# Kernel optimization log

Measured on AMD Instinct MI355X. Metric: run time of the kernel, lower is better.

## Reference

```python
import jax, jax.numpy as jnp
import numpy as np

MAX_P = 20
MAX_N = 50
FDIM = 256
SCALE = 0.08
STEPS = 3


def _grid_sample_border(feat_hwc, grid):
    # feat_hwc: [B,H,W,C]; grid: [B,Q,2] normalized xy in [-1,1]
    # Bilinear grid_sample, padding_mode='border', align_corners=False (matches torch).
    B, H, W, C = feat_hwc.shape

    def one(fm, g):  # fm [H,W,C], g [Q,2]
        ix = jnp.clip(((g[:, 0] + 1.0) * W - 1.0) * 0.5, 0.0, W - 1.0)
        iy = jnp.clip(((g[:, 1] + 1.0) * H - 1.0) * 0.5, 0.0, H - 1.0)
        x0f = jnp.floor(ix); y0f = jnp.floor(iy)
        wx = (ix - x0f)[:, None]; wy = (iy - y0f)[:, None]
        x0 = x0f.astype(jnp.int32); y0 = y0f.astype(jnp.int32)
        x1 = jnp.minimum(x0 + 1, W - 1); y1 = jnp.minimum(y0 + 1, H - 1)
        f00 = fm[y0, x0]; f01 = fm[y0, x1]  # [Q,C]
        f10 = fm[y1, x0]; f11 = fm[y1, x1]
        top = f00 * (1.0 - wx) + f01 * wx
        bot = f10 * (1.0 - wx) + f11 * wx
        return top * (1.0 - wy) + bot * wy

    return jax.vmap(one)(feat_hwc, grid)


def setup_inputs() -> dict:
    key = jax.random.key(0)
    ks = jax.random.split(key, 12)
    d = {
        'p2': jax.random.normal(ks[0], (4, 256, 256, 256), jnp.float32),
        'p4': jax.random.normal(ks[1], (4, 256, 64, 64), jnp.float32),
        'iw1': jax.random.normal(ks[2], (16384, 512), jnp.float32) * 0.01,
        'ib1': jnp.zeros((512,), jnp.float32),
        'iw2': jax.random.normal(ks[3], (512, 1024), jnp.float32) * 0.04,
        'ib2': jnp.zeros((1024,), jnp.float32),
        'iw3': jax.random.normal(ks[4], (1024, 2000), jnp.float32) * 0.03,
        'ib3': jnp.zeros((2000,), jnp.float32),
        'rw1': jax.random.normal(ks[5], (258, 256), jnp.float32) * 0.06,
        'rb1': jnp.zeros((256,), jnp.float32),
        'rw2': jax.random.normal(ks[6], (256, 128), jnp.float32) * 0.06,
        'rb2': jnp.zeros((128,), jnp.float32),
        'rw3': jax.random.normal(ks[7], (128, 2), jnp.float32) * 0.09,
        'rb3': jnp.zeros((2,), jnp.float32),
        'vw1': jax.random.normal(ks[8], (100, 128), jnp.float32) * 0.1,
        'vb1': jnp.zeros((128,), jnp.float32),
        'vw2': jax.random.normal(ks[9], (128, 1), jnp.float32) * 0.09,
        'vb2': jnp.zeros((1,), jnp.float32),
    }
    return d


def reference(p2, p4, iw1, ib1, iw2, ib2, iw3, ib3,
              rw1, rb1, rw2, rb2, rw3, rb3, vw1, vb1, vw2, vb2):
    B = p4.shape[0]
    # AdaptiveAvgPool2d(8) on 64x64 -> mean over 8x8 blocks
    pooled = p4.reshape(B, FDIM, 8, 8, 8, 8).mean(axis=(3, 5))  # [B,C,8,8]
    flat = pooled.reshape(B, -1)  # [B, C*64]
    h = jax.nn.relu(flat @ iw1 + ib1)
    h = jax.nn.relu(h @ iw2 + ib2)
    init_polygons = jax.nn.sigmoid(h @ iw3 + ib3).reshape(B, MAX_P, MAX_N, 2)

    feat_hwc = jnp.transpose(p2, (0, 2, 3, 1))  # [B,H,W,C]
    polygons = init_polygons
    for _ in range(STEPS):
        coords = polygons.reshape(B, -1, 2)           # [B,Q,2] in [0,1]
        grid = coords * 2.0 - 1.0
        sampled = _grid_sample_border(feat_hwc, grid)  # [B,Q,C]
        inp = jnp.concatenate([sampled, coords], axis=-1)  # [B,Q,C+2]
        r = jax.nn.relu(inp @ rw1 + rb1)
        r = jax.nn.relu(r @ rw2 + rb2)
        disp = jnp.tanh(r @ rw3 + rb3).reshape(B, MAX_P, MAX_N, 2)
        bad = ~jnp.all(jnp.isfinite(disp))
        disp = jnp.where(bad, 0.0,
                         jnp.clip(disp * SCALE, -2.0 * SCALE, 2.0 * SCALE))
        polygons = jnp.clip(polygons + disp, 0.0, 1.0)

    poly_flat = polygons.reshape(B * MAX_P, MAX_N * 2)
    v = jax.nn.relu(poly_flat @ vw1 + vb1)
    validity = jax.nn.sigmoid(v @ vw2 + vb2).reshape(B, MAX_P)
    return polygons, validity, init_polygons
```

## Files before the change

kernel.cpp:

```cpp
#include <hip/hip_runtime.h>
#include <hip/hip_fp16.h>
#include <math.h>

#define WS_FLAT 0
#define WS_PART 65536
#define WS_H1   (65536 + 524288)
#define WS_H2   (WS_H1 + 2048)
#define WS_POLY (WS_H2 + 4096)
#define WS_P2T  1048576

__global__ void __launch_bounds__(256) transpose_k(const float* __restrict__ in,
                                                   __half* __restrict__ out) {
    __shared__ float t[64][65];
    int tile = blockIdx.x;
    int b  = tile >> 12;
    int ct = (tile >> 10) & 3;
    int xt = tile & 1023;
    int c0 = ct << 6, yx0 = xt << 6;
    int tid = threadIdx.x;

    int jv = (tid & 15) << 2;
    int i0 = tid >> 4;
    const float* ip = in + (((size_t)(b * 256 + c0)) << 16) + yx0;
    #pragma unroll
    for (int ii = i0; ii < 64; ii += 16) {
        float4 v = *(const float4*)(ip + ((size_t)ii << 16) + jv);
        t[jv + 0][ii] = v.x; t[jv + 1][ii] = v.y;
        t[jv + 2][ii] = v.z; t[jv + 3][ii] = v.w;
    }
    __syncthreads();

    int cl = (tid & 7) << 3;
    #pragma unroll
    for (int jj = tid >> 3; jj < 64; jj += 32) {
        union { __half h[8]; float4 f; } u;
        #pragma unroll
        for (int q = 0; q < 8; ++q) u.h[q] = __float2half(t[jj][cl + q]);
        *(float4*)(out + ((size_t)b << 24) + ((size_t)(yx0 + jj) << 8) + c0 + cl) = u.f;
    }
}

__global__ void pool_k(const float* __restrict__ p4, float* __restrict__ flat) {
    int o = blockIdx.x * blockDim.x + threadIdx.x;
    int b = o >> 14;
    int c = (o >> 6) & 255;
    int ij = o & 63;
    int i = ij >> 3, j = ij & 7;
    const float* base = p4 + (((size_t)(b * 256 + c) * 64 + i * 8) * 64 + j * 8);
    float s = 0.f;
    #pragma unroll
    for (int u = 0; u < 8; ++u) {
        const float4* r = (const float4*)(base + u * 64);
        float4 a = r[0], bb = r[1];
        s += a.x + a.y + a.z + a.w + bb.x + bb.y + bb.z + bb.w;
    }
    flat[o] = s * (1.0f / 64.0f);
}

__global__ void g1a_k(const float* __restrict__ flat, const float* __restrict__ iw1,
                      float* __restrict__ part) {
    __shared__ float sf[4][64];
    int tid = threadIdx.x;
    int kbase = blockIdx.x * 64;
    if (tid < 256) sf[tid >> 6][tid & 63] = flat[(tid >> 6) * 16384 + kbase + (tid & 63)];
    __syncthreads();
    float a0 = 0.f, a1 = 0.f, a2 = 0.f, a3 = 0.f;
    for (int k = 0; k < 64; ++k) {
        float w = iw1[(size_t)(kbase + k) * 512 + tid];
        a0 = fmaf(sf[0][k], w, a0);
        a1 = fmaf(sf[1][k], w, a1);
        a2 = fmaf(sf[2][k], w, a2);
        a3 = fmaf(sf[3][k], w, a3);
    }
    float* pp = part + (size_t)blockIdx.x * 2048;
    pp[tid] = a0; pp[512 + tid] = a1; pp[1024 + tid] = a2; pp[1536 + tid] = a3;
}

__global__ void g1b_k(const float* __restrict__ part, const float* __restrict__ ib1,
                      float* __restrict__ h1) {
    __shared__ float red[8][32];
    int tid = threadIdx.x;
    int cc = tid >> 5, oo = tid & 31;
    int o = blockIdx.x * 32 + oo;
    float s = 0.f;
    for (int i = 0; i < 32; ++i)
        s += part[(size_t)(cc + 8 * i) * 2048 + o];
    red[cc][oo] = s;
    __syncthreads();
    if (cc == 0) {
        float t = 0.f;
        #pragma unroll
        for (int c2 = 0; c2 < 8; ++c2) t += red[c2][oo];
        t += ib1[o & 511];
        h1[o] = fmaxf(t, 0.f);
    }
}

__global__ void g2_k(const float* __restrict__ h1, const float* __restrict__ iw2,
                     const float* __restrict__ ib2, float* __restrict__ h2) {
    __shared__ float sh[512];
    __shared__ float red[4][64];
    int tid = threadIdx.x;
    int b = blockIdx.x >> 4, jt = blockIdx.x & 15;
    sh[tid] = h1[b * 512 + tid];
    sh[tid + 256] = h1[b * 512 + 256 + tid];
    __syncthreads();
    int j = (jt << 6) + (tid & 63);
    int kc = tid >> 6;
    float acc = 0.f;
    for (int k = kc * 128; k < kc * 128 + 128; ++k)
        acc = fmaf(sh[k], iw2[(size_t)k * 1024 + j], acc);
    red[kc][tid & 63] = acc;
    __syncthreads();
    if (kc == 0) {
        float t = red[0][tid] + red[1][tid] + red[2][tid] + red[3][tid] + ib2[j];
        h2[b * 1024 + j] = fmaxf(t, 0.f);
    }
}

__global__ void g3_k(const float* __restrict__ h2, const float* __restrict__ iw3,
                     const float* __restrict__ ib3, float* __restrict__ out_init,
                     float* __restrict__ poly) {
    __shared__ float sh[1024];
    __shared__ float red[4][64];
    int tid = threadIdx.x;
    int b = blockIdx.x >> 5, jt = blockIdx.x & 31;
    const float* h = h2 + b * 1024;
    sh[tid] = h[tid]; sh[tid + 256] = h[tid + 256];
    sh[tid + 512] = h[tid + 512]; sh[tid + 768] = h[tid + 768];
    __syncthreads();
    int j = (jt << 6) + (tid & 63);
    int kc = tid >> 6;
    float acc = 0.f;
    if (j < 2000) {
        for (int k = kc * 256; k < kc * 256 + 256; ++k)
            acc = fmaf(sh[k], iw3[(size_t)k * 2000 + j], acc);
    }
    red[kc][tid & 63] = acc;
    __syncthreads();
    if (kc == 0 && j < 2000) {
        float t = red[0][tid] + red[1][tid] + red[2][tid] + red[3][tid] + ib3[j];
        float s = 1.f / (1.f + expf(-t));
        int o = b * 2000 + j;
        out_init[o] = s;
        poly[o] = s;
    }
}

__global__ void __launch_bounds__(256) step_k(
    const __half* __restrict__ p2th,
    const float* __restrict__ rw1, const float* __restrict__ rb1,
    const float* __restrict__ rw2, const float* __restrict__ rb2,
    const float* __restrict__ rw3, const float* __restrict__ rb3,
    float* __restrict__ poly) {
    __shared__ __align__(16) float s_inp[258 * 16];
    __shared__ __align__(16) float s_r1[256 * 16];
    __shared__ __align__(16) float s_r2[128 * 16];
    int tid = threadIdx.x;
    int pt0 = blockIdx.x * 16;

    {
        int ch2 = (tid & 127) << 1;
        int pgg = tid >> 7;
        float v0[8], v1[8];
        #pragma unroll
        for (int pp = 0; pp < 8; ++pp) {
            int pt = pt0 + pgg * 8 + pp;
            int b = pt / 1000;
            float cx = poly[pt * 2], cy = poly[pt * 2 + 1];
            float ix = fminf(fmaxf(cx * 256.f - 0.5f, 0.f), 255.f);
            float iy = fminf(fmaxf(cy * 256.f - 0.5f, 0.f), 255.f);
            float x0f = floorf(ix), y0f = floorf(iy);
            int x0 = (int)x0f, y0 = (int)y0f;
            int x1 = min(x0 + 1, 255), y1 = min(y0 + 1, 255);
            float wx = ix - x0f, wy = iy - y0f;
            const __half* bt = p2th + ((size_t)b << 24);
            int r0 = (y0 << 16) + (x0 << 8) + ch2;
            int r1a = (y1 << 16) + (x0 << 8) + ch2;
            int dx = (x1 - x0) << 8;
            float2 f00 = __half22float2(*(const __half2*)(bt + r0));
            float2 f01 = __half22float2(*(const __half2*)(bt + r0 + dx));
            float2 f10 = __half22float2(*(const __half2*)(bt + r1a));
            float2 f11 = __half22float2(*(const __half2*)(bt + r1a + dx));
            float t0 = f00.x + (f01.x - f00.x) * wx;
            float b0 = f10.x + (f11.x - f10.x) * wx;
            float t1 = f00.y + (f01.y - f00.y) * wx;
            float b1 = f10.y + (f11.y - f10.y) * wx;
            v0[pp] = t0 + (b0 - t0) * wy;
            v1[pp] = t1 + (b1 - t1) * wy;
        }
        float* r0p = &s_inp[ch2 * 16 + pgg * 8];
        float* r1p = &s_inp[(ch2 + 1) * 16 + pgg * 8];
        ((float4*)r0p)[0] = make_float4(v0[0], v0[1], v0[2], v0[3]);
        ((float4*)r0p)[1] = make_float4(v0[4], v0[5], v0[6], v0[7]);
        ((float4*)r1p)[0] = make_float4(v1[0], v1[1], v1[2], v1[3]);
        ((float4*)r1p)[1] = make_float4(v1[4], v1[5], v1[6], v1[7]);
        if (tid < 32) {
            int p = tid >> 1, d = tid & 1;
            s_inp[(256 + d) * 16 + p] = poly[(pt0 + p) * 2 + d];
        }
    }
    __syncthreads();

    int jc = tid & 63, pg = tid >> 6;
    {
        float4 bias = *(const float4*)(rb1 + jc * 4);
        float4 acc0 = bias, acc1 = bias, acc2 = bias, acc3 = bias;
        for (int k = 0; k < 258; ++k) {
            float4 a = *(const float4*)&s_inp[k * 16 + pg * 4];
            float4 w = *(const float4*)(rw1 + k * 256 + jc * 4);
            acc0.x = fmaf(a.x, w.x, acc0.x); acc0.y = fmaf(a.x, w.y, acc0.y);
            acc0.z = fmaf(a.x, w.z, acc0.z); acc0.w = fmaf(a.x, w.w, acc0.w);
            acc1.x = fmaf(a.y, w.x, acc1.x); acc1.y = fmaf(a.y, w.y, acc1.y);
            acc1.z = fmaf(a.y, w.z, acc1.z); acc1.w = fmaf(a.y, w.w, acc1.w);
            acc2.x = fmaf(a.z, w.x, acc2.x); acc2.y = fmaf(a.z, w.y, acc2.y);
            acc2.z = fmaf(a.z, w.z, acc2.z); acc2.w = fmaf(a.z, w.w, acc2.w);
            acc3.x = fmaf(a.w, w.x, acc3.x); acc3.y = fmaf(a.w, w.y, acc3.y);
            acc3.z = fmaf(a.w, w.z, acc3.z); acc3.w = fmaf(a.w, w.w, acc3.w);
        }
        acc0.x = fmaxf(acc0.x, 0.f); acc0.y = fmaxf(acc0.y, 0.f);
        acc0.z = fmaxf(acc0.z, 0.f); acc0.w = fmaxf(acc0.w, 0.f);
        acc1.x = fmaxf(acc1.x, 0.f); acc1.y = fmaxf(acc1.y, 0.f);
        acc1.z = fmaxf(acc1.z, 0.f); acc1.w = fmaxf(acc1.w, 0.f);
        acc2.x = fmaxf(acc2.x, 0.f); acc2.y = fmaxf(acc2.y, 0.f);
        acc2.z = fmaxf(acc2.z, 0.f); acc2.w = fmaxf(acc2.w, 0.f);
        acc3.x = fmaxf(acc3.x, 0.f); acc3.y = fmaxf(acc3.y, 0.f);
        acc3.z = fmaxf(acc3.z, 0.f); acc3.w = fmaxf(acc3.w, 0.f);
        *(float4*)&s_r1[(jc * 4 + 0) * 16 + pg * 4] = make_float4(acc0.x, acc1.x, acc2.x, acc3.x);
        *(float4*)&s_r1[(jc * 4 + 1) * 16 + pg * 4] = make_float4(acc0.y, acc1.y, acc2.y, acc3.y);
        *(float4*)&s_r1[(jc * 4 + 2) * 16 + pg * 4] = make_float4(acc0.z, acc1.z, acc2.z, acc3.z);
        *(float4*)&s_r1[(jc * 4 + 3) * 16 + pg * 4] = make_float4(acc0.w, acc1.w, acc2.w, acc3.w);
    }
    __syncthreads();

    {
        float2 bias = *(const float2*)(rb2 + jc * 2);
        float2 d0 = bias, d1 = bias, d2 = bias, d3 = bias;
        for (int k = 0; k < 256; ++k) {
            float4 a = *(const float4*)&s_r1[k * 16 + pg * 4];
            float2 w = *(const float2*)(rw2 + k * 128 + jc * 2);
            d0.x = fmaf(a.x, w.x, d0.x); d0.y = fmaf(a.x, w.y, d0.y);
            d1.x = fmaf(a.y, w.x, d1.x); d1.y = fmaf(a.y, w.y, d1.y);
            d2.x = fmaf(a.z, w.x, d2.x); d2.y = fmaf(a.z, w.y, d2.y);
            d3.x = fmaf(a.w, w.x, d3.x); d3.y = fmaf(a.w, w.y, d3.y);
        }
        d0.x = fmaxf(d0.x, 0.f); d0.y = fmaxf(d0.y, 0.f);
        d1.x = fmaxf(d1.x, 0.f); d1.y = fmaxf(d1.y, 0.f);
        d2.x = fmaxf(d2.x, 0.f); d2.y = fmaxf(d2.y, 0.f);
        d3.x = fmaxf(d3.x, 0.f); d3.y = fmaxf(d3.y, 0.f);
        *(float4*)&s_r2[(jc * 2 + 0) * 16 + pg * 4] = make_float4(d0.x, d1.x, d2.x, d3.x);
        *(float4*)&s_r2[(jc * 2 + 1) * 16 + pg * 4] = make_float4(d0.y, d1.y, d2.y, d3.y);
    }
    __syncthreads();

    if (tid < 32) {
        int p = tid >> 1, d = tid & 1;
        float acc = rb3[d];
        for (int k = 0; k < 128; ++k)
            acc = fmaf(s_r2[k * 16 + p], rw3[k * 2 + d], acc);
        float disp = tanhf(acc) * 0.08f;
        disp = fminf(fmaxf(disp, -0.16f), 0.16f);
        int idx = (pt0 + p) * 2 + d;
        float nv = poly[idx] + disp;
        poly[idx] = fminf(fmaxf(nv, 0.f), 1.f);
    }
}

__global__ void valid_k(const float* __restrict__ poly,
                        const float* __restrict__ vw1, const float* __restrict__ vb1,
                        const float* __restrict__ vw2, const float* __restrict__ vb2,
                        float* __restrict__ out) {
    __shared__ float sp[100];
    __shared__ float sred[2];
    int tid = threadIdx.x;
    int row = blockIdx.x;
    if (tid < 100) {
        float v = poly[row * 100 + tid];
        sp[tid] = v;
        out[row * 100 + tid] = v;
    }
    __syncthreads();
    float acc = vb1[tid];
    for (int k = 0; k < 100; ++k)
        acc = fmaf(sp[k], vw1[k * 128 + tid], acc);
    float pr = fmaxf(acc, 0.f) * vw2[tid];
    #pragma unroll
    for (int off = 32; off > 0; off >>= 1)
        pr += __shfl_down(pr, off, 64);
    if ((tid & 63) == 0) sred[tid >> 6] = pr;
    __syncthreads();
    if (tid == 0) {
        float s = sred[0] + sred[1] + vb2[0];
        out[8000 + row] = 1.f / (1.f + expf(-s));
    }
}

extern "C" void kernel_launch(void* const* d_in, const int* in_sizes, int n_in,
                              void* d_out, int out_size, void* d_ws, size_t ws_size,
                              hipStream_t stream) {
    const float* p2  = (const float*)d_in[0];
    const float* p4  = (const float*)d_in[1];
    const float* iw1 = (const float*)d_in[2];
    const float* ib1 = (const float*)d_in[3];
    const float* iw2 = (const float*)d_in[4];
    const float* ib2 = (const float*)d_in[5];
    const float* iw3 = (const float*)d_in[6];
    const float* ib3 = (const float*)d_in[7];
    const float* rw1 = (const float*)d_in[8];
    const float* rb1 = (const float*)d_in[9];
    const float* rw2 = (const float*)d_in[10];
    const float* rb2 = (const float*)d_in[11];
    const float* rw3 = (const float*)d_in[12];
    const float* rb3 = (const float*)d_in[13];
    const float* vw1 = (const float*)d_in[14];
    const float* vb1 = (const float*)d_in[15];
    const float* vw2 = (const float*)d_in[16];
    const float* vb2 = (const float*)d_in[17];
    float* out = (float*)d_out;
    float* ws = (float*)d_ws;
    float* flat = ws + WS_FLAT;
    float* part = ws + WS_PART;
    float* h1   = ws + WS_H1;
    float* h2   = ws + WS_H2;
    float* poly = ws + WS_POLY;
    __half* p2th = (__half*)(ws + WS_P2T);

    pool_k<<<256, 256, 0, stream>>>(p4, flat);
    g1a_k<<<256, 512, 0, stream>>>(flat, iw1, part);
    g1b_k<<<64, 256, 0, stream>>>(part, ib1, h1);
    g2_k<<<64, 256, 0, stream>>>(h1, iw2, ib2, h2);
    g3_k<<<128, 256, 0, stream>>>(h2, iw3, ib3, out + 8080, poly);
    transpose_k<<<16384, 256, 0, stream>>>(p2, p2th);
    for (int s = 0; s < 3; ++s)
        step_k<<<250, 256, 0, stream>>>(p2th, rw1, rb1, rw2, rb2, rw3, rb3, poly);
    valid_k<<<80, 128, 0, stream>>>(poly, vw1, vb1, vw2, vb2, out);
}
```

Baseline: 585.0 us.

## Fuse pooling into transpose kernel and halve points per refinement block

The p4 pooling work now runs as extra blocks appended to the p2 transpose/fp16 conversion kernel, which removes one launch and lets the small pooling job overlap with the large transpose. The refinement step kernel now handles 8 points per block instead of 16 and launches 500 blocks instead of 250. This spreads the work over more CUs on a GPU where 250 blocks underfill the device. Shared-memory layouts for the MLP intermediates are changed to row-per-point with padding. The cost is that each block reuses each weight load across fewer points, so more global or L2 weight traffic is needed per point.

```diff
diff --git a/kernel.cpp b/kernel.cpp
--- a/kernel.cpp
+++ b/kernel.cpp
@@ -9,52 +9,52 @@
 #define WS_POLY (WS_H2 + 4096)
 #define WS_P2T  1048576
 
-__global__ void __launch_bounds__(256) transpose_k(const float* __restrict__ in,
-                                                   __half* __restrict__ out) {
+__global__ void __launch_bounds__(256) fused0_k(const float* __restrict__ p2,
+                                                __half* __restrict__ p2th,
+                                                const float* __restrict__ p4,
+                                                float* __restrict__ flat) {
     __shared__ float t[64][65];
-    int tile = blockIdx.x;
-    int b  = tile >> 12;
-    int ct = (tile >> 10) & 3;
-    int xt = tile & 1023;
-    int c0 = ct << 6, yx0 = xt << 6;
-    int tid = threadIdx.x;
-
-    int jv = (tid & 15) << 2;
-    int i0 = tid >> 4;
-    const float* ip = in + (((size_t)(b * 256 + c0)) << 16) + yx0;
-    #pragma unroll
-    for (int ii = i0; ii < 64; ii += 16) {
-        float4 v = *(const float4*)(ip + ((size_t)ii << 16) + jv);
-        t[jv + 0][ii] = v.x; t[jv + 1][ii] = v.y;
-        t[jv + 2][ii] = v.z; t[jv + 3][ii] = v.w;
-    }
-    __syncthreads();
-
-    int cl = (tid & 7) << 3;
-    #pragma unroll
-    for (int jj = tid >> 3; jj < 64; jj += 32) {
-        union { __half h[8]; float4 f; } u;
-        #pragma unroll
-        for (int q = 0; q < 8; ++q) u.h[q] = __float2half(t[jj][cl + q]);
-        *(float4*)(out + ((size_t)b << 24) + ((size_t)(yx0 + jj) << 8) + c0 + cl) = u.f;
-    }
-}
-
-__global__ void pool_k(const float* __restrict__ p4, float* __restrict__ flat) {
-    int o = blockIdx.x * blockDim.x + threadIdx.x;
-    int b = o >> 14;
-    int c = (o >> 6) & 255;
-    int ij = o & 63;
-    int i = ij >> 3, j = ij & 7;
-    const float* base = p4 + (((size_t)(b * 256 + c) * 64 + i * 8) * 64 + j * 8);
-    float s = 0.f;
-    #pragma unroll
-    for (int u = 0; u < 8; ++u) {
-        const float4* r = (const float4*)(base + u * 64);
-        float4 a = r[0], bb = r[1];
-        s += a.x + a.y + a.z + a.w + bb.x + bb.y + bb.z + bb.w;
-    }
-    flat[o] = s * (1.0f / 64.0f);
+    int tid = threadIdx.x;
+    if (blockIdx.x < 16384) {
+        int tile = blockIdx.x;
+        int b  = tile >> 12;
+        int ct = (tile >> 10) & 3;
+        int xt = tile & 1023;
+        int c0 = ct << 6, yx0 = xt << 6;
+        int jv = (tid & 15) << 2;
+        int i0 = tid >> 4;
+        const float* ip = p2 + (((size_t)(b * 256 + c0)) << 16) + yx0;
+        #pragma unroll
+        for (int ii = i0; ii < 64; ii += 16) {
+            float4 v = *(const float4*)(ip + ((size_t)ii << 16) + jv);
+            t[jv + 0][ii] = v.x; t[jv + 1][ii] = v.y;
+            t[jv + 2][ii] = v.z; t[jv + 3][ii] = v.w;
+        }
+        __syncthreads();
+        int cl = (tid & 7) << 3;
+        #pragma unroll
+        for (int jj = tid >> 3; jj < 64; jj += 32) {
+            union { __half h[8]; float4 f; } u;
+            #pragma unroll
+            for (int q = 0; q < 8; ++q) u.h[q] = __float2half(t[jj][cl + q]);
+            *(float4*)(p2th + ((size_t)b << 24) + ((size_t)(yx0 + jj) << 8) + c0 + cl) = u.f;
+        }
+    } else {
+        int o = (blockIdx.x - 16384) * 256 + tid;
+        int b = o >> 14;
+        int c = (o >> 6) & 255;
+        int ij = o & 63;
+        int i = ij >> 3, j = ij & 7;
+        const float* base = p4 + (((size_t)(b * 256 + c) * 64 + i * 8) * 64 + j * 8);
+        float s = 0.f;
+        #pragma unroll
+        for (int u = 0; u < 8; ++u) {
+            const float4* r = (const float4*)(base + u * 64);
+            float4 a = r[0], bb = r[1];
+            s += a.x + a.y + a.z + a.w + bb.x + bb.y + bb.z + bb.w;
+        }
+        flat[o] = s * (1.0f / 64.0f);
+    }
 }
 
 __global__ void g1a_k(const float* __restrict__ flat, const float* __restrict__ iw1,
@@ -153,20 +153,21 @@
     const float* __restrict__ rw2, const float* __restrict__ rb2,
     const float* __restrict__ rw3, const float* __restrict__ rb3,
     float* __restrict__ poly) {
-    __shared__ __align__(16) float s_inp[258 * 16];
-    __shared__ __align__(16) float s_r1[256 * 16];
-    __shared__ __align__(16) float s_r2[128 * 16];
-    int tid = threadIdx.x;
-    int pt0 = blockIdx.x * 16;
+    __shared__ __align__(16) float s_inp[258 * 8];
+    __shared__ __align__(16) float s_r1[8 * 256];
+    __shared__ __align__(16) float s_r2[8 * 132];
+    int tid = threadIdx.x;
+    int pt0 = blockIdx.x * 8;
+    int b = pt0 / 1000;
+    const __half* bt = p2th + ((size_t)b << 24);
 
     {
         int ch2 = (tid & 127) << 1;
         int pgg = tid >> 7;
-        float v0[8], v1[8];
-        #pragma unroll
-        for (int pp = 0; pp < 8; ++pp) {
-            int pt = pt0 + pgg * 8 + pp;
-            int b = pt / 1000;
+        float v0[4], v1[4];
+        #pragma unroll
+        for (int pp = 0; pp < 4; ++pp) {
+            int pt = pt0 + pgg * 4 + pp;
             float cx = poly[pt * 2], cy = poly[pt * 2 + 1];
             float ix = fminf(fmaxf(cx * 256.f - 0.5f, 0.f), 255.f);
             float iy = fminf(fmaxf(cy * 256.f - 0.5f, 0.f), 255.f);
@@ -174,7 +175,6 @@
             int x0 = (int)x0f, y0 = (int)y0f;
             int x1 = min(x0 + 1, 255), y1 = min(y0 + 1, 255);
             float wx = ix - x0f, wy = iy - y0f;
-            const __half* bt = p2th + ((size_t)b << 24);
             int r0 = (y0 << 16) + (x0 << 8) + ch2;
             int r1a = (y1 << 16) + (x0 << 8) + ch2;
             int dx = (x1 - x0) << 8;
@@ -189,75 +189,60 @@
             v0[pp] = t0 + (b0 - t0) * wy;
             v1[pp] = t1 + (b1 - t1) * wy;
         }
-        float* r0p = &s_inp[ch2 * 16 + pgg * 8];
-        float* r1p = &s_inp[(ch2 + 1) * 16 + pgg * 8];
-        ((float4*)r0p)[0] = make_float4(v0[0], v0[1], v0[2], v0[3]);
-        ((float4*)r0p)[1] = make_float4(v0[4], v0[5], v0[6], v0[7]);
-        ((float4*)r1p)[0] = make_float4(v1[0], v1[1], v1[2], v1[3]);
-        ((float4*)r1p)[1] = make_float4(v1[4], v1[5], v1[6], v1[7]);
-        if (tid < 32) {
+        *(float4*)&s_inp[ch2 * 8 + pgg * 4] = make_float4(v0[0], v0[1], v0[2], v0[3]);
+        *(float4*)&s_inp[(ch2 + 1) * 8 + pgg * 4] = make_float4(v1[0], v1[1], v1[2], v1[3]);
+        if (tid < 16) {
             int p = tid >> 1, d = tid & 1;
-            s_inp[(256 + d) * 16 + p] = poly[(pt0 + p) * 2 + d];
+            s_inp[(256 + d) * 8 + p] = poly[(pt0 + p) * 2 + d];
         }
     }
     __syncthreads();
 
     int jc = tid & 63, pg = tid >> 6;
+
     {
         float4 bias = *(const float4*)(rb1 + jc * 4);
-        float4 acc0 = bias, acc1 = bias, acc2 = bias, acc3 = bias;
+        float4 accA = bias, accB = bias;
         for (int k = 0; k < 258; ++k) {
-            float4 a = *(const float4*)&s_inp[k * 16 + pg * 4];
+            float2 a = *(const float2*)&s_inp[k * 8 + pg * 2];
             float4 w = *(const float4*)(rw1 + k * 256 + jc * 4);
-            acc0.x = fmaf(a.x, w.x, acc0.x); acc0.y = fmaf(a.x, w.y, acc0.y);
-            acc0.z = fmaf(a.x, w.z, acc0.z); acc0.w = fmaf(a.x, w.w, acc0.w);
-            acc1.x = fmaf(a.y, w.x, acc1.x); acc1.y = fmaf(a.y, w.y, acc1.y);
-            acc1.z = fmaf(a.y, w.z, acc1.z); acc1.w = fmaf(a.y, w.w, acc1.w);
-            acc2.x = fmaf(a.z, w.x, acc2.x); acc2.y = fmaf(a.z, w.y, acc2.y);
-            acc2.z = fmaf(a.z, w.z, acc2.z); acc2.w = fmaf(a.z, w.w, acc2.w);
-            acc3.x = fmaf(a.w, w.x, acc3.x); acc3.y = fmaf(a.w, w.y, acc3.y);
-            acc3.z = fmaf(a.w, w.z, acc3.z); acc3.w = fmaf(a.w, w.w, acc3.w);
-        }
-        acc0.x = fmaxf(acc0.x, 0.f); acc0.y = fmaxf(acc0.y, 0.f);
-        acc0.z = fmaxf(acc0.z, 0.f); acc0.w = fmaxf(acc0.w, 0.f);
-        acc1.x = fmaxf(acc1.x, 0.f); acc1.y = fmaxf(acc1.y, 0.f);
-        acc1.z = fmaxf(acc1.z, 0.f); acc1.w = fmaxf(acc1.w, 0.f);
-        acc2.x = fmaxf(acc2.x, 0.f); acc2.y = fmaxf(acc2.y, 0.f);
-        acc2.z = fmaxf(acc2.z, 0.f); acc2.w = fmaxf(acc2.w, 0.f);
-        acc3.x = fmaxf(acc3.x, 0.f); acc3.y = fmaxf(acc3.y, 0.f);
-        acc3.z = fmaxf(acc3.z, 0.f); acc3.w = fmaxf(acc3.w, 0.f);
-        *(float4*)&s_r1[(jc * 4 + 0) * 16 + pg * 4] = make_float4(acc0.x, acc1.x, acc2.x, acc3.x);
-        *(float4*)&s_r1[(jc * 4 + 1) * 16 + pg * 4] = make_float4(acc0.y, acc1.y, acc2.y, acc3.y);
-        *(float4*)&s_r1[(jc * 4 + 2) * 16 + pg * 4] = make_float4(acc0.z, acc1.z, acc2.z, acc3.z);
-        *(float4*)&s_r1[(jc * 4 + 3) * 16 + pg * 4] = make_float4(acc0.w, acc1.w, acc2.w, acc3.w);
+            accA.x = fmaf(a.x, w.x, accA.x); accA.y = fmaf(a.x, w.y, accA.y);
+            accA.z = fmaf(a.x, w.z, accA.z); accA.w = fmaf(a.x, w.w, accA.w);
+            accB.x = fmaf(a.y, w.x, accB.x); accB.y = fmaf(a.y, w.y, accB.y);
+            accB.z = fmaf(a.y, w.z, accB.z); accB.w = fmaf(a.y, w.w, accB.w);
+        }
+        accA.x = fmaxf(accA.x, 0.f); accA.y = fmaxf(accA.y, 0.f);
+        accA.z = fmaxf(accA.z, 0.f); accA.w = fmaxf(accA.w, 0.f);
+        accB.x = fmaxf(accB.x, 0.f); accB.y = fmaxf(accB.y, 0.f);
+        accB.z = fmaxf(accB.z, 0.f); accB.w = fmaxf(accB.w, 0.f);
+        *(float4*)&s_r1[(pg * 2 + 0) * 256 + jc * 4] = accA;
+        *(float4*)&s_r1[(pg * 2 + 1) * 256 + jc * 4] = accB;
     }
     __syncthreads();
 
     {
+        const float* rA = &s_r1[(pg * 2 + 0) * 256];
+        const float* rB = &s_r1[(pg * 2 + 1) * 256];
         float2 bias = *(const float2*)(rb2 + jc * 2);
-        float2 d0 = bias, d1 = bias, d2 = bias, d3 = bias;
+        float2 dA = bias, dB = bias;
         for (int k = 0; k < 256; ++k) {
-            float4 a = *(const float4*)&s_r1[k * 16 + pg * 4];
+            float aA = rA[k], aB = rB[k];
             float2 w = *(const float2*)(rw2 + k * 128 + jc * 2);
-            d0.x = fmaf(a.x, w.x, d0.x); d0.y = fmaf(a.x, w.y, d0.y);
-            d1.x = fmaf(a.y, w.x, d1.x); d1.y = fmaf(a.y, w.y, d1.y);
-            d2.x = fmaf(a.z, w.x, d2.x); d2.y = fmaf(a.z, w.y, d2.y);
-            d3.x = fmaf(a.w, w.x, d3.x); d3.y = fmaf(a.w, w.y, d3.y);
-        }
-        d0.x = fmaxf(d0.x, 0.f); d0.y = fmaxf(d0.y, 0.f);
-        d1.x = fmaxf(d1.x, 0.f); d1.y = fmaxf(d1.y, 0.f);
-        d2.x = fmaxf(d2.x, 0.f); d2.y = fmaxf(d2.y, 0.f);
-        d3.x = fmaxf(d3.x, 0.f); d3.y = fmaxf(d3.y, 0.f);
-        *(float4*)&s_r2[(jc * 2 + 0) * 16 + pg * 4] = make_float4(d0.x, d1.x, d2.x, d3.x);
-        *(float4*)&s_r2[(jc * 2 + 1) * 16 + pg * 4] = make_float4(d0.y, d1.y, d2.y, d3.y);
-    }
-    __syncthreads();
-
-    if (tid < 32) {
+            dA.x = fmaf(aA, w.x, dA.x); dA.y = fmaf(aA, w.y, dA.y);
+            dB.x = fmaf(aB, w.x, dB.x); dB.y = fmaf(aB, w.y, dB.y);
+        }
+        dA.x = fmaxf(dA.x, 0.f); dA.y = fmaxf(dA.y, 0.f);
+        dB.x = fmaxf(dB.x, 0.f); dB.y = fmaxf(dB.y, 0.f);
+        *(float2*)&s_r2[(pg * 2 + 0) * 132 + jc * 2] = dA;
+        *(float2*)&s_r2[(pg * 2 + 1) * 132 + jc * 2] = dB;
+    }
+    __syncthreads();
+
+    if (tid < 16) {
         int p = tid >> 1, d = tid & 1;
         float acc = rb3[d];
         for (int k = 0; k < 128; ++k)
-            acc = fmaf(s_r2[k * 16 + p], rw3[k * 2 + d], acc);
+            acc = fmaf(s_r2[p * 132 + k], rw3[k * 2 + d], acc);
         float disp = tanhf(acc) * 0.08f;
         disp = fminf(fmaxf(disp, -0.16f), 0.16f);
         int idx = (pt0 + p) * 2 + d;
@@ -325,13 +310,12 @@
     float* poly = ws + WS_POLY;
     __half* p2th = (__half*)(ws + WS_P2T);
 
-    pool_k<<<256, 256, 0, stream>>>(p4, flat);
+    fused0_k<<<16640, 256, 0, stream>>>(p2, p2th, p4, flat);
     g1a_k<<<256, 512, 0, stream>>>(flat, iw1, part);
     g1b_k<<<64, 256, 0, stream>>>(part, ib1, h1);
     g2_k<<<64, 256, 0, stream>>>(h1, iw2, ib2, h2);
     g3_k<<<128, 256, 0, stream>>>(h2, iw3, ib3, out + 8080, poly);
-    transpose_k<<<16384, 256, 0, stream>>>(p2, p2th);
     for (int s = 0; s < 3; ++s)
-        step_k<<<250, 256, 0, stream>>>(p2th, rw1, rb1, rw2, rb2, rw3, rb3, poly);
+        step_k<<<500, 256, 0, stream>>>(p2th, rw1, rb1, rw2, rb2, rw3, rb3, poly);
     valid_k<<<80, 128, 0, stream>>>(poly, vw1, vb1, vw2, vb2, out);
 }
```

After: 605.3 us. 3.5% more time.
